# Performance work log

Measured on AMD Instinct MI355X. Metric: run time of the kernel, lower is better.

The kernel has to match this reference:

```python
import jax, jax.numpy as jnp
import numpy as np

EPS = 1e-08


def _l2norm(x):
    return x / (jnp.linalg.norm(x, axis=-1, keepdims=True) + EPS)


def _mlp(x, weights):
    # weights: list of (W, b); gelu between layers, none after last
    n = len(weights)
    for i, (W, b) in enumerate(weights):
        x = x @ W + b
        if i < n - 1:
            x = jax.nn.gelu(x)  # approximate gelu, matches jax.nn.gelu default
    return x


def setup_inputs() -> dict:
    key = jax.random.key(0)
    ks = jax.random.split(key, 16)
    N, A, L, K = 65536, 32, 256, 1024
    enc_dims = [A, 512, 1024, L]
    dec_dims = [L, 1024, 512, A]

    def lin(k, din, dout):
        kw, kb = jax.random.split(k)
        W = jax.random.normal(kw, (din, dout), jnp.float32) / np.sqrt(din)
        b = jnp.zeros((dout,), jnp.float32)
        return W, b

    inp = {}
    inp["action"] = jax.random.normal(ks[0], (N, A), jnp.float32)
    inp["dim_weights"] = jax.random.uniform(ks[1], (A,), jnp.float32)
    for i in range(3):
        W, b = lin(ks[2 + i], enc_dims[i], enc_dims[i + 1])
        inp[f"enc_w{i}"], inp[f"enc_b{i}"] = W, b
    for i in range(3):
        W, b = lin(ks[5 + i], dec_dims[i], dec_dims[i + 1])
        inp[f"dec_w{i}"], inp[f"dec_b{i}"] = W, b
    cb = jax.random.normal(ks[8], (K, L), jnp.float32) * 0.1
    inp["codebook"] = _l2norm(cb)
    return inp


def reference(action, dim_weights,
              enc_w0, enc_b0, enc_w1, enc_b1, enc_w2, enc_b2,
              dec_w0, dec_b0, dec_w1, dec_b1, dec_w2, dec_b2,
              codebook):
    enc = [(enc_w0, enc_b0), (enc_w1, enc_b1), (enc_w2, enc_b2)]
    dec = [(dec_w0, dec_b0), (dec_w1, dec_b1), (dec_w2, dec_b2)]

    z_e = _l2norm(_mlp(action, enc))                       # [N, L]
    cb = _l2norm(codebook)                                 # [K, L]
    # squared euclidean distances [N, K]
    dists = (jnp.sum(z_e * z_e, axis=-1, keepdims=True)
             - 2.0 * z_e @ cb.T
             + jnp.sum(cb * cb, axis=-1))
    code_idx = jnp.argmin(dists, axis=-1)                  # [N]
    z_q = cb[code_idx]                                     # [N, L]

    z_q_ste = z_e + jax.lax.stop_gradient(z_q - z_e)
    action_hat = _mlp(z_q_ste, dec)                        # [N, A]

    sq_err = (action - action_hat) ** 2 * dim_weights
    recon_loss = jnp.mean(sq_err)
    codebook_loss = jnp.mean((jax.lax.stop_gradient(z_e) - z_q) ** 2)
    commit_loss = jnp.mean((z_e - jax.lax.stop_gradient(z_q)) ** 2)
    return action_hat, code_idx, recon_loss, codebook_loss, commit_loss
```

## Files before the change

kernel.cpp:

```cpp
#include <hip/hip_runtime.h>
#include <math.h>

#define N_ROWS 65536

typedef short short8 __attribute__((ext_vector_type(8)));
typedef float f32x4 __attribute__((ext_vector_type(4)));

__device__ __forceinline__ float gelu_f(float x) {
  float x3 = x * x * x;
  float t = tanhf(0.7978845608028654f * (x + 0.044715f * x3));
  return 0.5f * x * (1.0f + t);
}

__device__ __forceinline__ unsigned short f2bf(float f) {
  unsigned u = __float_as_uint(f);
  unsigned r = u + 0x7fffu + ((u >> 16) & 1u);
  return (unsigned short)(r >> 16);
}
__device__ __forceinline__ float bf2f(unsigned short h) {
  return __uint_as_float(((unsigned)h) << 16);
}

__device__ __forceinline__ void split3(float v, unsigned short& p0,
                                       unsigned short& p1, unsigned short& p2) {
  p0 = f2bf(v);
  float r = v - bf2f(p0);
  p1 = f2bf(r);
  r -= bf2f(p1);
  p2 = f2bf(r);
}

__device__ __forceinline__ void split3f(float v, unsigned short& p0,
                                        unsigned short& p1, unsigned short& p2) {
  unsigned u = __float_as_uint(v);
  unsigned h0 = (u + 0x8000u) & 0xffff0000u;
  float r = v - __uint_as_float(h0);
  unsigned u1 = __float_as_uint(r);
  unsigned h1 = (u1 + 0x8000u) & 0xffff0000u;
  float r2 = r - __uint_as_float(h1);
  p0 = (unsigned short)(h0 >> 16);
  p1 = (unsigned short)(h1 >> 16);
  p2 = f2bf(r2);
}

__device__ __forceinline__ void split2f(float v, unsigned short& p0,
                                        unsigned short& p1) {
  unsigned u = __float_as_uint(v);
  unsigned h0 = (u + 0x8000u) & 0xffff0000u;
  float r = v - __uint_as_float(h0);
  p0 = (unsigned short)(h0 >> 16);
  p1 = f2bf(r);
}

__device__ __forceinline__ f32x4 mfma16(short8 a, short8 b, f32x4 c) {
  return __builtin_amdgcn_mfma_f32_16x16x32_bf16(a, b, c, 0, 0, 0);
}

__global__ __launch_bounds__(256) void gemm_enc0_split(
    const float* __restrict__ A, const float* __restrict__ W,
    const float* __restrict__ bias, unsigned short* __restrict__ P,
    size_t aps, int din, int dout) {
  __shared__ float As[16][132];
  __shared__ float Ws[16][132];
  int t = threadIdx.x;
  int tx = t & 15, ty = t >> 4;
  int c0 = blockIdx.x * 128;
  int r0 = blockIdx.y * 128;

  float acc[8][8];
#pragma unroll
  for (int i = 0; i < 8; ++i)
#pragma unroll
    for (int j = 0; j < 8; ++j) acc[i][j] = 0.0f;

  int kchunks = din >> 4;
  for (int kc = 0; kc < kchunks; ++kc) {
    int k0 = kc << 4;
    __syncthreads();
#pragma unroll
    for (int it = 0; it < 2; ++it) {
      int id = t + it * 256;
      int r = id >> 2;
      int kq = (id & 3) * 4;
      float4 v = *(const float4*)&A[(long)(r0 + r) * din + (k0 + kq)];
      As[kq + 0][r] = v.x; As[kq + 1][r] = v.y;
      As[kq + 2][r] = v.z; As[kq + 3][r] = v.w;
      int k = id >> 5;
      int cq = (id & 31) * 4;
      float4 w = *(const float4*)&W[(long)(k0 + k) * dout + (c0 + cq)];
      *(float4*)&Ws[k][cq] = w;
    }
    __syncthreads();
#pragma unroll
    for (int k = 0; k < 16; ++k) {
      float av[8], bv[8];
      *(float4*)&av[0] = *(const float4*)&As[k][ty * 4];
      *(float4*)&av[4] = *(const float4*)&As[k][ty * 4 + 64];
      *(float4*)&bv[0] = *(const float4*)&Ws[k][tx * 4];
      *(float4*)&bv[4] = *(const float4*)&Ws[k][tx * 4 + 64];
#pragma unroll
      for (int i = 0; i < 8; ++i)
#pragma unroll
        for (int j = 0; j < 8; ++j)
          acc[i][j] = fmaf(av[i], bv[j], acc[i][j]);
    }
  }

  float bbv[8];
  *(float4*)&bbv[0] = *(const float4*)&bias[c0 + tx * 4];
  *(float4*)&bbv[4] = *(const float4*)&bias[c0 + tx * 4 + 64];
#pragma unroll
  for (int i = 0; i < 8; ++i) {
    long row = r0 + ty * 4 + (i & 3) + ((i >> 2) * 64);
    unsigned short s0[8], s1[8], s2[8];
#pragma unroll
    for (int j = 0; j < 8; ++j) {
      float v = gelu_f(acc[i][j] + bbv[j]);
      split3f(v, s0[j], s1[j], s2[j]);
    }
    size_t b = (size_t)row * dout + c0 + tx * 4;
    ushort4 w;
    w.x = s0[0]; w.y = s0[1]; w.z = s0[2]; w.w = s0[3];
    *(ushort4*)&P[b] = w;
    w.x = s0[4]; w.y = s0[5]; w.z = s0[6]; w.w = s0[7];
    *(ushort4*)&P[b + 64] = w;
    w.x = s1[0]; w.y = s1[1]; w.z = s1[2]; w.w = s1[3];
    *(ushort4*)&P[aps + b] = w;
    w.x = s1[4]; w.y = s1[5]; w.z = s1[6]; w.w = s1[7];
    *(ushort4*)&P[aps + b + 64] = w;
    w.x = s2[0]; w.y = s2[1]; w.z = s2[2]; w.w = s2[3];
    *(ushort4*)&P[2 * aps + b] = w;
    w.x = s2[4]; w.y = s2[5]; w.z = s2[6]; w.w = s2[7];
    *(ushort4*)&P[2 * aps + b + 64] = w;
  }
}

template <bool GELU>
__global__ __launch_bounds__(256) void gemm64_kernel(
    const float* __restrict__ A, const float* __restrict__ W,
    const float* __restrict__ bias, float* __restrict__ C,
    int din, int dout) {
  __shared__ float As[16][68];
  __shared__ float Ws[16][68];
  int t = threadIdx.x;
  int tx = t & 15, ty = t >> 4;
  int c0 = blockIdx.x * 64;
  int r0 = blockIdx.y * 64;

  float acc[4][4];
#pragma unroll
  for (int i = 0; i < 4; ++i)
#pragma unroll
    for (int j = 0; j < 4; ++j) acc[i][j] = 0.0f;

  int kchunks = din >> 4;
  for (int kc = 0; kc < kchunks; ++kc) {
    int k0 = kc << 4;
    __syncthreads();
    {
      int r = t >> 2, kq = (t & 3) * 4;
      float4 v = *(const float4*)&A[(long)(r0 + r) * din + (k0 + kq)];
      As[kq + 0][r] = v.x; As[kq + 1][r] = v.y;
      As[kq + 2][r] = v.z; As[kq + 3][r] = v.w;
      int k = t >> 4, cq = (t & 15) * 4;
      *(float4*)&Ws[k][cq] = *(const float4*)&W[(long)(k0 + k) * dout + (c0 + cq)];
    }
    __syncthreads();
#pragma unroll
    for (int k = 0; k < 16; ++k) {
      float av[4], bv[4];
      *(float4*)&av[0] = *(const float4*)&As[k][ty * 4];
      *(float4*)&bv[0] = *(const float4*)&Ws[k][tx * 4];
#pragma unroll
      for (int i = 0; i < 4; ++i)
#pragma unroll
        for (int j = 0; j < 4; ++j)
          acc[i][j] = fmaf(av[i], bv[j], acc[i][j]);
    }
  }

  float4 bb = *(const float4*)&bias[c0 + tx * 4];
#pragma unroll
  for (int i = 0; i < 4; ++i) {
    long row = r0 + ty * 4 + i;
    float o[4];
    o[0] = acc[i][0] + bb.x; o[1] = acc[i][1] + bb.y;
    o[2] = acc[i][2] + bb.z; o[3] = acc[i][3] + bb.w;
    if (GELU) {
      o[0] = gelu_f(o[0]); o[1] = gelu_f(o[1]);
      o[2] = gelu_f(o[2]); o[3] = gelu_f(o[3]);
    }
    *(float4*)&C[row * dout + c0 + tx * 4] = *(float4*)&o[0];
  }
}

__global__ void frag_pack_kernel(const float* __restrict__ W,
                                 unsigned short* __restrict__ Bf,
                                 int K, int N) {
  int l = threadIdx.x;
  int m = l & 15, q = l >> 4;
  int cb = blockIdx.x, kb = blockIdx.y;
  unsigned short s0[8], s1[8], s2[8];
#pragma unroll
  for (int j = 0; j < 8; ++j) {
    float v = W[(long)(kb * 32 + q * 8 + j) * N + cb * 16 + m];
    split3(v, s0[j], s1[j], s2[j]);
  }
  size_t base = ((size_t)cb * (K / 32) + kb) * 3 * 512;
  *(short8*)&Bf[base + 0 * 512 + l * 8] = *(short8*)s0;
  *(short8*)&Bf[base + 1 * 512 + l * 8] = *(short8*)s1;
  *(short8*)&Bf[base + 2 * 512 + l * 8] = *(short8*)s2;
}

__global__ void frag_pack2_t(const float* __restrict__ cbn,
                             unsigned short* __restrict__ Bf) {
  int l = threadIdx.x;
  int m = l & 15, q = l >> 4;
  int cb = blockIdx.x, kb = blockIdx.y;
  unsigned short s0[8], s1[8];
  const float* src = cbn + (long)(cb * 16 + m) * 256 + kb * 32 + q * 8;
#pragma unroll
  for (int j = 0; j < 8; ++j) split2f(src[j], s0[j], s1[j]);
  size_t base = ((size_t)(cb * 8 + kb) * 2) * 512;
  *(short8*)&Bf[base + l * 8] = *(short8*)s0;
  *(short8*)&Bf[base + 512 + l * 8] = *(short8*)s1;
}

template <bool GELU>
__global__ __launch_bounds__(256) void mfma3_gemm(
    const unsigned short* __restrict__ Ap, size_t aps,
    const unsigned short* __restrict__ Bf,
    const float* __restrict__ bias, float* __restrict__ C,
    int K, int dout) {
  __shared__ unsigned short A_f[2][3 * 2 * 4 * 512];
  int t = threadIdx.x;
  int lane = t & 63, wave = t >> 6;
  int q = lane >> 4, m = lane & 15;
  int wrb = wave >> 1;
  int wr = wrb * 64, wc = (wave & 1) * 64;

  int gx = gridDim.x, tot = gx * gridDim.y;
  int lin = blockIdx.y * gx + blockIdx.x;
  if (!(tot & 7)) lin = (lin & 7) * (tot >> 3) + (lin >> 3);
  int bx = lin % gx, by = lin / gx;

  long r0 = (long)by * 128;
  int c0 = bx * 128;
  int kchunks = K >> 5;

  f32x4 acc[4][4];
#pragma unroll
  for (int i = 0; i < 4; ++i)
#pragma unroll
    for (int j = 0; j < 4; ++j) acc[i][j] = (f32x4){0.f, 0.f, 0.f, 0.f};

  int rs = t >> 1, hs = (t & 1) * 16;
  const unsigned short* a0p = Ap + (size_t)(r0 + rs) * K + hs;
  const unsigned short* a1p = a0p + aps;
  const unsigned short* a2p = a0p + 2 * aps;
  int cb0 = (c0 + wc) >> 4;
  int xw = (rs >> 4) & 3, wrbw = rs >> 6, mw = rs & 15;
  int g0 = ((t & 1) * 2 + 0) * 16 + mw;
  int g1 = ((t & 1) * 2 + 1) * 16 + mw;
  int wb0 = (0 * 2 + wrbw) * 4 + xw;
  int wb1 = (1 * 2 + wrbw) * 4 + xw;
  int wb2 = (2 * 2 + wrbw) * 4 + xw;

  {
    uint4 u00 = *(const uint4*)(a0p);
    uint4 u01 = *(const uint4*)(a0p + 8);
    uint4 u10 = *(const uint4*)(a1p);
    uint4 u11 = *(const uint4*)(a1p + 8);
    uint4 u20 = *(const uint4*)(a2p);
    uint4 u21 = *(const uint4*)(a2p + 8);
    *(uint4*)&A_f[0][wb0 * 512 + g0 * 8] = u00;
    *(uint4*)&A_f[0][wb0 * 512 + g1 * 8] = u01;
    *(uint4*)&A_f[0][wb1 * 512 + g0 * 8] = u10;
    *(uint4*)&A_f[0][wb1 * 512 + g1 * 8] = u11;
    *(uint4*)&A_f[0][wb2 * 512 + g0 * 8] = u20;
    *(uint4*)&A_f[0][wb2 * 512 + g1 * 8] = u21;
  }
  __syncthreads();

  int cur = 0;
  for (int kb = 0; kb < kchunks; ++kb) {
    short8 af[3][4];
#pragma unroll
    for (int p = 0; p < 3; ++p)
#pragma unroll
      for (int x = 0; x < 4; ++x)
        af[p][x] =
            *(const short8*)&A_f[cur][((p * 2 + wrb) * 4 + x) * 512 + lane * 8];
#pragma unroll
    for (int ct = 0; ct < 4; ++ct) {
      size_t fb = ((size_t)(cb0 + ct) * kchunks + kb) * 3 * 512 + lane * 8;
      short8 b0 = *(const short8*)&Bf[fb];
      short8 b1 = *(const short8*)&Bf[fb + 512];
      short8 b2 = *(const short8*)&Bf[fb + 1024];
#pragma unroll
      for (int rt = 0; rt < 4; ++rt) {
        acc[rt][ct] = mfma16(af[0][rt], b0, acc[rt][ct]);
        acc[rt][ct] = mfma16(af[0][rt], b1, acc[rt][ct]);
        acc[rt][ct] = mfma16(af[1][rt], b0, acc[rt][ct]);
        acc[rt][ct] = mfma16(af[0][rt], b2, acc[rt][ct]);
        acc[rt][ct] = mfma16(af[1][rt], b1, acc[rt][ct]);
        acc[rt][ct] = mfma16(af[2][rt], b0, acc[rt][ct]);
      }
    }
    if (kb + 1 < kchunks) {
      int kt = (kb + 1) << 5;
      uint4 u00 = *(const uint4*)(a0p + kt);
      uint4 u01 = *(const uint4*)(a0p + kt + 8);
      uint4 u10 = *(const uint4*)(a1p + kt);
      uint4 u11 = *(const uint4*)(a1p + kt + 8);
      uint4 u20 = *(const uint4*)(a2p + kt);
      uint4 u21 = *(const uint4*)(a2p + kt + 8);
      int nb = cur ^ 1;
      *(uint4*)&A_f[nb][wb0 * 512 + g0 * 8] = u00;
      *(uint4*)&A_f[nb][wb0 * 512 + g1 * 8] = u01;
      *(uint4*)&A_f[nb][wb1 * 512 + g0 * 8] = u10;
      *(uint4*)&A_f[nb][wb1 * 512 + g1 * 8] = u11;
      *(uint4*)&A_f[nb][wb2 * 512 + g0 * 8] = u20;
      *(uint4*)&A_f[nb][wb2 * 512 + g1 * 8] = u21;
    }
    __syncthreads();
    cur ^= 1;
  }

#pragma unroll
  for (int ct = 0; ct < 4; ++ct) {
    long col = c0 + wc + ct * 16 + m;
    float bv = bias[col];
#pragma unroll
    for (int rt = 0; rt < 4; ++rt) {
      long rowb = r0 + wr + rt * 16 + q * 4;
#pragma unroll
      for (int r = 0; r < 4; ++r) {
        float v = acc[rt][ct][r] + bv;
        if (GELU) v = gelu_f(v);
        C[(rowb + r) * dout + col] = v;
      }
    }
  }
}

__global__ __launch_bounds__(256) void mfma3_norm(
    const float* __restrict__ A, const unsigned short* __restrict__ Bf,
    const float* __restrict__ bias, float* __restrict__ z_e,
    float* __restrict__ ze2) {
  __shared__ unsigned short A_f[2][3 * 4 * 512];
  __shared__ float S[64][4];
  __shared__ float Sinv[64];
  const int K = 1024, kchunks = 32;
  int t = threadIdx.x;
  int lane = t & 63, wave = t >> 6;
  int q = lane >> 4, m = lane & 15;
  long r0 = (long)blockIdx.x * 64;

  f32x4 acc[4][4];
#pragma unroll
  for (int i = 0; i < 4; ++i)
#pragma unroll
    for (int j = 0; j < 4; ++j) acc[i][j] = (f32x4){0.f, 0.f, 0.f, 0.f};

  int rs = t >> 2, kq = t & 3;
  const float* aptr = A + (r0 + rs) * K + kq * 8;
  int xw = rs >> 4, mw = rs & 15;
  int gw = kq * 16 + mw;
  int wb0 = 0 * 4 + xw, wb1 = 1 * 4 + xw, wb2 = 2 * 4 + xw;
  int cb0 = wave * 4;

  {
    float fv[8];
    *(float4*)&fv[0] = *(const float4*)(aptr);
    *(float4*)&fv[4] = *(const float4*)(aptr + 4);
    unsigned short a0[8], a1[8], a2[8];
#pragma unroll
    for (int i = 0; i < 8; ++i) split3f(fv[i], a0[i], a1[i], a2[i]);
    *(uint4*)&A_f[0][wb0 * 512 + gw * 8] = *(uint4*)a0;
    *(uint4*)&A_f[0][wb1 * 512 + gw * 8] = *(uint4*)a1;
    *(uint4*)&A_f[0][wb2 * 512 + gw * 8] = *(uint4*)a2;
  }
  __syncthreads();

  int cur = 0;
  for (int kb = 0; kb < kchunks; ++kb) {
    short8 af[3][4];
#pragma unroll
    for (int p = 0; p < 3; ++p)
#pragma unroll
      for (int x = 0; x < 4; ++x)
        af[p][x] = *(const short8*)&A_f[cur][(p * 4 + x) * 512 + lane * 8];
#pragma unroll
    for (int ct = 0; ct < 4; ++ct) {
      size_t fb = ((size_t)(cb0 + ct) * kchunks + kb) * 3 * 512 + lane * 8;
      short8 b0 = *(const short8*)&Bf[fb];
      short8 b1 = *(const short8*)&Bf[fb + 512];
      short8 b2 = *(const short8*)&Bf[fb + 1024];
#pragma unroll
      for (int rt = 0; rt < 4; ++rt) {
        acc[rt][ct] = mfma16(af[0][rt], b0, acc[rt][ct]);
        acc[rt][ct] = mfma16(af[0][rt], b1, acc[rt][ct]);
        acc[rt][ct] = mfma16(af[1][rt], b0, acc[rt][ct]);
        acc[rt][ct] = mfma16(af[0][rt], b2, acc[rt][ct]);
        acc[rt][ct] = mfma16(af[1][rt], b1, acc[rt][ct]);
        acc[rt][ct] = mfma16(af[2][rt], b0, acc[rt][ct]);
      }
    }
    if (kb + 1 < kchunks) {
      float fv[8];
      *(float4*)&fv[0] = *(const float4*)(aptr + ((kb + 1) << 5));
      *(float4*)&fv[4] = *(const float4*)(aptr + ((kb + 1) << 5) + 4);
      unsigned short a0[8], a1[8], a2[8];
#pragma unroll
      for (int i = 0; i < 8; ++i) split3f(fv[i], a0[i], a1[i], a2[i]);
      int nb = cur ^ 1;
      *(uint4*)&A_f[nb][wb0 * 512 + gw * 8] = *(uint4*)a0;
      *(uint4*)&A_f[nb][wb1 * 512 + gw * 8] = *(uint4*)a1;
      *(uint4*)&A_f[nb][wb2 * 512 + gw * 8] = *(uint4*)a2;
    }
    __syncthreads();
    cur ^= 1;
  }

#pragma unroll
  for (int ct = 0; ct < 4; ++ct) {
    float bv = bias[wave * 64 + ct * 16 + m];
#pragma unroll
    for (int rt = 0; rt < 4; ++rt)
#pragma unroll
      for (int r = 0; r < 4; ++r) acc[rt][ct][r] += bv;
  }

#pragma unroll
  for (int rt = 0; rt < 4; ++rt)
#pragma unroll
    for (int r = 0; r < 4; ++r) {
      float s = acc[rt][0][r] * acc[rt][0][r] + acc[rt][1][r] * acc[rt][1][r] +
                acc[rt][2][r] * acc[rt][2][r] + acc[rt][3][r] * acc[rt][3][r];
#pragma unroll
      for (int off = 1; off <= 8; off <<= 1) s += __shfl_xor(s, off);
      if (m == 0) S[rt * 16 + q * 4 + r][wave] = s;
    }
  __syncthreads();
  if (t < 64) {
    float s = S[t][0] + S[t][1] + S[t][2] + S[t][3];
    float den = sqrtf(s) + 1e-8f;
    Sinv[t] = 1.0f / den;
    ze2[r0 + t] = s / (den * den);
  }
  __syncthreads();
#pragma unroll
  for (int rt = 0; rt < 4; ++rt)
#pragma unroll
    for (int r = 0; r < 4; ++r) {
      int rl = rt * 16 + q * 4 + r;
      float inv = Sinv[rl];
#pragma unroll
      for (int ct = 0; ct < 4; ++ct)
        z_e[(r0 + rl) * 256 + wave * 64 + ct * 16 + m] = acc[rt][ct][r] * inv;
    }
}

__global__ __launch_bounds__(256) void dist2_mfma(
    const float* __restrict__ z_e, const unsigned short* __restrict__ cbf,
    int* __restrict__ idxc, int* __restrict__ fixcnt, int* __restrict__ fixlist) {
  __shared__ unsigned short A_f[2 * 8 * 4 * 512];
  __shared__ float Lv1[64][4], Lv2[64][4];
  __shared__ int Lc1[64][4];
  int t = threadIdx.x;
  int lane = t & 63, wave = t >> 6;
  int q = lane >> 4, m = lane & 15;
  long r0 = (long)blockIdx.x * 64;

#pragma unroll
  for (int it = 0; it < 4; ++it) {
    int kb = it * 2 + (t >> 7);
    int rs = (t & 127) >> 1, hs = (t & 1) * 16;
    const float* ap = z_e + (r0 + rs) * 256 + kb * 32 + hs;
    float fv[16];
    *(float4*)&fv[0] = *(const float4*)(ap + 0);
    *(float4*)&fv[4] = *(const float4*)(ap + 4);
    *(float4*)&fv[8] = *(const float4*)(ap + 8);
    *(float4*)&fv[12] = *(const float4*)(ap + 12);
    unsigned short a0[16], a1[16];
#pragma unroll
    for (int i = 0; i < 16; ++i) split2f(fv[i], a0[i], a1[i]);
    int x = rs >> 4, mm = rs & 15;
    int ga = ((t & 1) * 2 + 0) * 16 + mm;
    int gb = ((t & 1) * 2 + 1) * 16 + mm;
    int b0 = ((0 * 8 + kb) * 4 + x) * 512;
    int b1 = ((1 * 8 + kb) * 4 + x) * 512;
    *(uint4*)&A_f[b0 + ga * 8] = ((uint4*)a0)[0];
    *(uint4*)&A_f[b0 + gb * 8] = ((uint4*)a0)[1];
    *(uint4*)&A_f[b1 + ga * 8] = ((uint4*)a1)[0];
    *(uint4*)&A_f[b1 + gb * 8] = ((uint4*)a1)[1];
  }
  __syncthreads();

  float v1[4][4], v2[4][4];
  int c1[4][4];
#pragma unroll
  for (int i = 0; i < 4; ++i)
#pragma unroll
    for (int j = 0; j < 4; ++j) { v1[i][j] = -3.4e38f; v2[i][j] = -3.4e38f; c1[i][j] = 0; }

  for (int ctp = 0; ctp < 4; ++ctp) {
    f32x4 acc[4][4];
#pragma unroll
    for (int i = 0; i < 4; ++i)
#pragma unroll
      for (int j = 0; j < 4; ++j) acc[i][j] = (f32x4){0.f, 0.f, 0.f, 0.f};

    for (int kb = 0; kb < 8; ++kb) {
      short8 af0[4], af1[4];
#pragma unroll
      for (int rt = 0; rt < 4; ++rt) {
        af0[rt] = *(const short8*)&A_f[((0 * 8 + kb) * 4 + rt) * 512 + lane * 8];
        af1[rt] = *(const short8*)&A_f[((1 * 8 + kb) * 4 + rt) * 512 + lane * 8];
      }
      short8 bf0[4], bf1[4];
#pragma unroll
      for (int cs = 0; cs < 4; ++cs) {
        int cb = ctp * 16 + (cs >> 1) * 8 + wave * 2 + (cs & 1);
        size_t fb = ((size_t)(cb * 8 + kb) * 2) * 512 + lane * 8;
        bf0[cs] = *(const short8*)&cbf[fb];
        bf1[cs] = *(const short8*)&cbf[fb + 512];
      }
#pragma unroll
      for (int rt = 0; rt < 4; ++rt)
#pragma unroll
        for (int cs = 0; cs < 4; ++cs) {
          acc[rt][cs] = mfma16(af0[rt], bf0[cs], acc[rt][cs]);
          acc[rt][cs] = mfma16(af0[rt], bf1[cs], acc[rt][cs]);
          acc[rt][cs] = mfma16(af1[rt], bf0[cs], acc[rt][cs]);
        }
    }
#pragma unroll
    for (int rt = 0; rt < 4; ++rt)
#pragma unroll
      for (int cs = 0; cs < 4; ++cs) {
        int colb = ctp * 256 + (cs >> 1) * 128 + wave * 32 + (cs & 1) * 16 + m;
#pragma unroll
        for (int r = 0; r < 4; ++r) {
          float v = acc[rt][cs][r];
          float nv2 = fmaxf(v2[rt][r], fminf(v, v1[rt][r]));
          if (v > v1[rt][r]) { c1[rt][r] = colb; v1[rt][r] = v; }
          v2[rt][r] = nv2;
        }
      }
  }

#pragma unroll
  for (int off = 1; off <= 8; off <<= 1) {
#pragma unroll
    for (int rt = 0; rt < 4; ++rt)
#pragma unroll
      for (int r = 0; r < 4; ++r) {
        float ov1 = __shfl_xor(v1[rt][r], off);
        float ov2 = __shfl_xor(v2[rt][r], off);
        int oc1 = __shfl_xor(c1[rt][r], off);
        float nv2 = fmaxf(fmaxf(v2[rt][r], ov2), fminf(v1[rt][r], ov1));
        if (ov1 > v1[rt][r] || (ov1 == v1[rt][r] && oc1 < c1[rt][r])) {
          v1[rt][r] = ov1; c1[rt][r] = oc1;
        }
        v2[rt][r] = nv2;
      }
  }
  if (m == 0) {
#pragma unroll
    for (int rt = 0; rt < 4; ++rt)
#pragma unroll
      for (int r = 0; r < 4; ++r) {
        int rloc = rt * 16 + q * 4 + r;
        Lv1[rloc][wave] = v1[rt][r];
        Lv2[rloc][wave] = v2[rt][r];
        Lc1[rloc][wave] = c1[rt][r];
      }
  }
  __syncthreads();
  if (t < 64) {
    float a1 = Lv1[t][0], a2 = Lv2[t][0];
    int ac = Lc1[t][0];
#pragma unroll
    for (int w = 1; w < 4; ++w) {
      float b1 = Lv1[t][w], b2 = Lv2[t][w];
      int bc = Lc1[t][w];
      float n2 = fmaxf(fmaxf(a2, b2), fminf(a1, b1));
      if (b1 > a1 || (b1 == a1 && bc < ac)) { a1 = b1; ac = bc; }
      a2 = n2;
    }
    idxc[r0 + t] = ac;
    if (a1 - a2 < 5.0e-4f) {
      int p = atomicAdd(fixcnt, 1);
      fixlist[p] = r0 + t;
    }
  }
}

__global__ __launch_bounds__(256) void fixup_part(
    const float* __restrict__ z_e, const float* __restrict__ cbn,
    const float* __restrict__ ze2, const float* __restrict__ cb2,
    const int* __restrict__ fixlist, const int* __restrict__ fixcnt,
    float* __restrict__ fixbv, int* __restrict__ fixbc) {
  int cnt = *fixcnt;
  int r0 = blockIdx.y * 128;
  if (r0 >= cnt) return;
  int ctile = blockIdx.x;
  int c0 = ctile * 128;
  __shared__ float As[16][132];
  __shared__ float Ws[16][132];
  __shared__ float rv[128][17];
  __shared__ int rc[128][17];
  __shared__ int rows_l[128];
  int t = threadIdx.x, tx = t & 15, ty = t >> 4;

  if (t < 128) rows_l[t] = fixlist[(r0 + t < cnt) ? (r0 + t) : 0];
  __syncthreads();

  float bestv[8];
  int bestc[8];
  float myze2[8];
#pragma unroll
  for (int i = 0; i < 8; ++i) {
    bestv[i] = 3.4e38f;
    bestc[i] = 0;
    int rl = ty * 4 + (i & 3) + ((i >> 2) * 64);
    myze2[i] = ze2[rows_l[rl]];
  }

  float acc[8][8];
#pragma unroll
  for (int i = 0; i < 8; ++i)
#pragma unroll
    for (int j = 0; j < 8; ++j) acc[i][j] = 0.0f;

  for (int kc = 0; kc < 16; ++kc) {
    int k0 = kc << 4;
    __syncthreads();
#pragma unroll
    for (int it = 0; it < 2; ++it) {
      int id = t + it * 256;
      int r = id >> 2;
      int kq = (id & 3) * 4;
      float4 v = *(const float4*)&z_e[(long)rows_l[r] * 256 + k0 + kq];
      As[kq + 0][r] = v.x; As[kq + 1][r] = v.y;
      As[kq + 2][r] = v.z; As[kq + 3][r] = v.w;
      float4 w = *(const float4*)&cbn[(long)(c0 + r) * 256 + k0 + kq];
      Ws[kq + 0][r] = w.x; Ws[kq + 1][r] = w.y;
      Ws[kq + 2][r] = w.z; Ws[kq + 3][r] = w.w;
    }
    __syncthreads();
#pragma unroll
    for (int k = 0; k < 16; ++k) {
      float av[8], bv[8];
      *(float4*)&av[0] = *(const float4*)&As[k][ty * 4];
      *(float4*)&av[4] = *(const float4*)&As[k][ty * 4 + 64];
      *(float4*)&bv[0] = *(const float4*)&Ws[k][tx * 4];
      *(float4*)&bv[4] = *(const float4*)&Ws[k][tx * 4 + 64];
#pragma unroll
      for (int i = 0; i < 8; ++i)
#pragma unroll
        for (int j = 0; j < 8; ++j)
          acc[i][j] = fmaf(av[i], bv[j], acc[i][j]);
    }
  }

  float cb2v[8];
  *(float4*)&cb2v[0] = *(const float4*)&cb2[c0 + tx * 4];
  *(float4*)&cb2v[4] = *(const float4*)&cb2[c0 + tx * 4 + 64];
#pragma unroll
  for (int i = 0; i < 8; ++i)
#pragma unroll
    for (int j = 0; j < 8; ++j) {
      int c = c0 + tx * 4 + (j & 3) + ((j >> 2) * 64);
      float d = (myze2[i] - 2.0f * acc[i][j]) + cb2v[j];
      if (d < bestv[i] || (d == bestv[i] && c < bestc[i])) {
        bestv[i] = d;
        bestc[i] = c;
      }
    }

  __syncthreads();
#pragma unroll
  for (int i = 0; i < 8; ++i) {
    int rl = ty * 4 + (i & 3) + ((i >> 2) * 64);
    rv[rl][tx] = bestv[i];
    rc[rl][tx] = bestc[i];
  }
  __syncthreads();
  if (t < 128 && r0 + t < cnt) {
    float bv = rv[t][0];
    int bc = rc[t][0];
    for (int j = 1; j < 16; ++j) {
      float v = rv[t][j];
      int c = rc[t][j];
      if (v < bv || (v == bv && c < bc)) { bv = v; bc = c; }
    }
    fixbv[(long)(r0 + t) * 8 + ctile] = bv;
    fixbc[(long)(r0 + t) * 8 + ctile] = bc;
  }
}

__global__ __launch_bounds__(256) void fixup_reduce(
    const float* __restrict__ fixbv, const int* __restrict__ fixbc,
    const int* __restrict__ fixlist, const int* __restrict__ fixcnt,
    int* __restrict__ idxc) {
  int cnt = *fixcnt;
  int i = blockIdx.x * 256 + threadIdx.x;
  if (i >= cnt) return;
  float bv = fixbv[(long)i * 8];
  int bc = fixbc[(long)i * 8];
#pragma unroll
  for (int j = 1; j < 8; ++j) {
    float v = fixbv[(long)i * 8 + j];
    int c = fixbc[(long)i * 8 + j];
    if (v < bv || (v == bv && c < bc)) { bv = v; bc = c; }
  }
  idxc[fixlist[i]] = bc;
}

__global__ __launch_bounds__(256) void rownorm_kernel(
    const float* __restrict__ in, float* __restrict__ outv,
    float* __restrict__ outsq) {
  int wid = threadIdx.x >> 6, lane = threadIdx.x & 63;
  long row = (long)blockIdx.x * 4 + wid;
  const float* src = in + row * 256;
  float4 v = *(const float4*)&src[lane * 4];
  float s = v.x * v.x + v.y * v.y + v.z * v.z + v.w * v.w;
#pragma unroll
  for (int off = 32; off >= 1; off >>= 1) s += __shfl_xor(s, off);
  float denom = sqrtf(s) + 1e-8f;
  float4 o;
  o.x = v.x / denom; o.y = v.y / denom; o.z = v.z / denom; o.w = v.w / denom;
  *(float4*)&outv[row * 256 + lane * 4] = o;
  float s2 = o.x * o.x + o.y * o.y + o.z * o.z + o.w * o.w;
#pragma unroll
  for (int off = 32; off >= 1; off >>= 1) s2 += __shfl_xor(s2, off);
  if (lane == 0) outsq[row] = s2;
}

__global__ __launch_bounds__(256) void t2_kernel(
    const float* __restrict__ T1, const float* __restrict__ W,
    const float* __restrict__ bias, float* __restrict__ T2) {
  int id = blockIdx.x * 256 + threadIdx.x;
  int row = id >> 5, col = id & 31;
  const float* a = T1 + (long)row * 512;
  float s = 0.f;
#pragma unroll 8
  for (int k = 0; k < 512; ++k) s = fmaf(a[k], W[k * 32 + col], s);
  T2[id] = s + bias[col];
}

__global__ __launch_bounds__(256) void fused_tail(
    const float* __restrict__ z_e, const float* __restrict__ cbn,
    const int* __restrict__ idxc, const float* __restrict__ T2,
    const float* __restrict__ action, const float* __restrict__ dimw,
    float* __restrict__ partRe, float* __restrict__ partCo,
    float* __restrict__ outIdx, float* __restrict__ ahat, int pb) {
  int t = threadIdx.x, wid = t >> 6, lane = t & 63;
  float cs = 0.f, rsum = 0.f;
#pragma unroll
  for (int r = 0; r < 4; ++r) {
    long row = (long)blockIdx.x * 16 + wid * 4 + r;
    int k = idxc[row];
    float4 a = *(const float4*)&z_e[row * 256 + lane * 4];
    float4 b = *(const float4*)&cbn[(long)k * 256 + lane * 4];
    float dx = a.x - b.x, dy = a.y - b.y, dz = a.z - b.z, dq = a.w - b.w;
    cs += dx * dx + dy * dy + dz * dz + dq * dq;
    if (lane < 8) {
      float4 av = *(const float4*)&action[row * 32 + lane * 4];
      float4 tv = *(const float4*)&T2[(long)k * 32 + lane * 4];
      float4 wv = *(const float4*)&dimw[lane * 4];
      *(float4*)&ahat[row * 32 + lane * 4] = tv;
      float ex = av.x - tv.x, ey = av.y - tv.y;
      float ez = av.z - tv.z, ew = av.w - tv.w;
      rsum += ex * ex * wv.x + ey * ey * wv.y + ez * ez * wv.z + ew * ew * wv.w;
    }
    if (lane == 0) outIdx[row] = (float)k;
  }
#pragma unroll
  for (int off = 32; off >= 1; off >>= 1) {
    cs += __shfl_xor(cs, off);
    rsum += __shfl_xor(rsum, off);
  }
  __shared__ float rc[4], rr[4];
  if (lane == 0) { rc[wid] = cs; rr[wid] = rsum; }
  __syncthreads();
  if (t == 0) {
    partCo[pb + blockIdx.x] = rc[0] + rc[1] + rc[2] + rc[3];
    partRe[pb + blockIdx.x] = rr[0] + rr[1] + rr[2] + rr[3];
  }
}

__global__ void zero_kernel(int* __restrict__ cnts) {
  if (threadIdx.x < 32) cnts[threadIdx.x] = 0;
}

__global__ __launch_bounds__(256) void finalize_kernel(
    const float* __restrict__ partRe, const float* __restrict__ partCo,
    float* __restrict__ out) {
  int t = threadIdx.x;
  float sr = 0.f, sc = 0.f;
  for (int i = t; i < 4096; i += 256) { sr += partRe[i]; sc += partCo[i]; }
#pragma unroll
  for (int off = 32; off >= 1; off >>= 1) {
    sr += __shfl_xor(sr, off);
    sc += __shfl_xor(sc, off);
  }
  __shared__ float rs_[4], cs_[4];
  int wid = t >> 6, lane = t & 63;
  if (lane == 0) { rs_[wid] = sr; cs_[wid] = sc; }
  __syncthreads();
  if (t == 0) {
    float r = rs_[0] + rs_[1] + rs_[2] + rs_[3];
    float c = cs_[0] + cs_[1] + cs_[2] + cs_[3];
    out[0] = r / (65536.0f * 32.0f);
    float cl = c / (65536.0f * 256.0f);
    out[1] = cl;
    out[2] = cl;
  }
}

extern "C" void kernel_launch(void* const* d_in, const int* in_sizes, int n_in,
                              void* d_out, int out_size, void* d_ws,
                              size_t ws_size, hipStream_t stream) {
  const float* action = (const float*)d_in[0];
  const float* dimw = (const float*)d_in[1];
  const float* ew0 = (const float*)d_in[2];
  const float* eb0 = (const float*)d_in[3];
  const float* ew1 = (const float*)d_in[4];
  const float* eb1 = (const float*)d_in[5];
  const float* ew2 = (const float*)d_in[6];
  const float* eb2 = (const float*)d_in[7];
  const float* dw0 = (const float*)d_in[8];
  const float* db0 = (const float*)d_in[9];
  const float* dw1 = (const float*)d_in[10];
  const float* db1 = (const float*)d_in[11];
  const float* dw2 = (const float*)d_in[12];
  const float* db2 = (const float*)d_in[13];
  const float* cb = (const float*)d_in[14];
  float* out = (float*)d_out;
  char* ws = (char*)d_ws;

  const size_t fixed_b = 1048576 + 4096 + 1048576 + 3145728 + 1572864 +
                         4194304 + 2097152 + 131072 + 256 + 32768;
  int R = N_ROWS;
  while (R > 2048) {
    if (fixed_b + (size_t)R * 7244 + 65536 <= ws_size) break;
    R >>= 1;
  }

  size_t off = 0;
  float* cbn = (float*)(ws + off); off += 1048576;
  float* cb2 = (float*)(ws + off); off += 4096;
  unsigned short* cbf = (unsigned short*)(ws + off); off += 1048576;
  unsigned short* ewf1 = (unsigned short*)(ws + off); off += 3145728;
  unsigned short* ewf2 = (unsigned short*)(ws + off); off += 1572864;
  float* T0 = (float*)(ws + off); off += 4194304;
  float* T1d = (float*)(ws + off); off += 2097152;
  float* T2d = (float*)(ws + off); off += 131072;
  int* fixcnts = (int*)(ws + off); off += 256;
  float* partRe = (float*)(ws + off); off += 16384;
  float* partCo = (float*)(ws + off); off += 16384;
  float* ze2 = (float*)(ws + off); off += (size_t)R * 4;
  int* idxc = (int*)(ws + off); off += (size_t)R * 4;
  int* fixlist = (int*)(ws + off); off += (size_t)R * 4;
  float* fixbv = (float*)(ws + off); off += (size_t)R * 32;
  int* fixbc = (int*)(ws + off); off += (size_t)R * 32;
  char* P0 = ws + off; off += (size_t)R * 3072;
  char* P1 = ws + off; off += (size_t)R * 4096;

  unsigned short* e0p = (unsigned short*)P0;
  size_t aps0 = (size_t)R * 512;
  float* e1 = (float*)P1;
  float* z_e = (float*)P0;

  zero_kernel<<<1, 64, 0, stream>>>(fixcnts);
  rownorm_kernel<<<256, 256, 0, stream>>>(cb, cbn, cb2);
  frag_pack2_t<<<dim3(64, 8), 64, 0, stream>>>(cbn, cbf);
  frag_pack_kernel<<<dim3(64, 16), 64, 0, stream>>>(ew1, ewf1, 512, 1024);
  frag_pack_kernel<<<dim3(16, 32), 64, 0, stream>>>(ew2, ewf2, 1024, 256);

  gemm64_kernel<true><<<dim3(16, 16), 256, 0, stream>>>(cbn, dw0, db0, T0, 256, 1024);
  gemm64_kernel<true><<<dim3(8, 16), 256, 0, stream>>>(T0, dw1, db1, T1d, 1024, 512);
  t2_kernel<<<128, 256, 0, stream>>>(T1d, dw2, db2, T2d);

  for (int base = 0; base < N_ROWS; base += R) {
    int ci = base / R;
    const float* act_c = action + (size_t)base * 32;
    float* out_c = out + (size_t)base * 32;
    int* fixcnt = &fixcnts[ci];

    gemm_enc0_split<<<dim3(4, R / 128), 256, 0, stream>>>(
        act_c, ew0, eb0, e0p, aps0, 32, 512);
    mfma3_gemm<true><<<dim3(8, R / 128), 256, 0, stream>>>(
        e0p, aps0, ewf1, eb1, e1, 512, 1024);
    mfma3_norm<<<R / 64, 256, 0, stream>>>(e1, ewf2, eb2, z_e, ze2);

    dist2_mfma<<<R / 64, 256, 0, stream>>>(z_e, cbf, idxc, fixcnt, fixlist);
    fixup_part<<<dim3(8, R / 128), 256, 0, stream>>>(
        z_e, cbn, ze2, cb2, fixlist, fixcnt, fixbv, fixbc);
    fixup_reduce<<<R / 256, 256, 0, stream>>>(fixbv, fixbc, fixlist, fixcnt,
                                              idxc);

    fused_tail<<<R / 16, 256, 0, stream>>>(
        z_e, cbn, idxc, T2d, act_c, dimw, partRe, partCo,
        out + 2097152 + base, out_c, base >> 4);
  }

  finalize_kernel<<<1, 256, 0, stream>>>(partRe, partCo, out + 2162688);
}
```

Baseline: 1.126 ms.

## Prefetch next B fragment in MFMA GEMMs and run VQ stages once over all rows

```diff
diff --git a/kernel.cpp b/kernel.cpp
--- a/kernel.cpp
+++ b/kernel.cpp
@@ -266,6 +266,13 @@
   int wb1 = (1 * 2 + wrbw) * 4 + xw;
   int wb2 = (2 * 2 + wrbw) * 4 + xw;
 
+  short8 pf0, pf1, pf2;
+  {
+    size_t fb = ((size_t)cb0 * kchunks) * 1536 + lane * 8;
+    pf0 = *(const short8*)&Bf[fb];
+    pf1 = *(const short8*)&Bf[fb + 512];
+    pf2 = *(const short8*)&Bf[fb + 1024];
+  }
   {
     uint4 u00 = *(const uint4*)(a0p);
     uint4 u01 = *(const uint4*)(a0p + 8);
@@ -292,8 +299,23 @@
         af[p][x] =
             *(const short8*)&A_f[cur][((p * 2 + wrb) * 4 + x) * 512 + lane * 8];
 #pragma unroll
-    for (int ct = 0; ct < 4; ++ct) {
-      size_t fb = ((size_t)(cb0 + ct) * kchunks + kb) * 3 * 512 + lane * 8;
+    for (int rt = 0; rt < 4; ++rt) {
+      acc[rt][0] = mfma16(af[0][rt], pf0, acc[rt][0]);
+      acc[rt][0] = mfma16(af[0][rt], pf1, acc[rt][0]);
+      acc[rt][0] = mfma16(af[1][rt], pf0, acc[rt][0]);
+      acc[rt][0] = mfma16(af[0][rt], pf2, acc[rt][0]);
+      acc[rt][0] = mfma16(af[1][rt], pf1, acc[rt][0]);
+      acc[rt][0] = mfma16(af[2][rt], pf0, acc[rt][0]);
+    }
+    if (kb + 1 < kchunks) {
+      size_t fb = ((size_t)cb0 * kchunks + kb + 1) * 1536 + lane * 8;
+      pf0 = *(const short8*)&Bf[fb];
+      pf1 = *(const short8*)&Bf[fb + 512];
+      pf2 = *(const short8*)&Bf[fb + 1024];
+    }
+#pragma unroll
+    for (int ct = 1; ct < 4; ++ct) {
+      size_t fb = ((size_t)(cb0 + ct) * kchunks + kb) * 1536 + lane * 8;
       short8 b0 = *(const short8*)&Bf[fb];
       short8 b1 = *(const short8*)&Bf[fb + 512];
       short8 b2 = *(const short8*)&Bf[fb + 1024];
@@ -370,6 +392,13 @@
   int wb0 = 0 * 4 + xw, wb1 = 1 * 4 + xw, wb2 = 2 * 4 + xw;
   int cb0 = wave * 4;
 
+  short8 pf0, pf1, pf2;
+  {
+    size_t fb = ((size_t)cb0 * kchunks) * 1536 + lane * 8;
+    pf0 = *(const short8*)&Bf[fb];
+    pf1 = *(const short8*)&Bf[fb + 512];
+    pf2 = *(const short8*)&Bf[fb + 1024];
+  }
   {
     float fv[8];
     *(float4*)&fv[0] = *(const float4*)(aptr);
@@ -392,8 +421,23 @@
       for (int x = 0; x < 4; ++x)
         af[p][x] = *(const short8*)&A_f[cur][(p * 4 + x) * 512 + lane * 8];
 #pragma unroll
-    for (int ct = 0; ct < 4; ++ct) {
-      size_t fb = ((size_t)(cb0 + ct) * kchunks + kb) * 3 * 512 + lane * 8;
+    for (int rt = 0; rt < 4; ++rt) {
+      acc[rt][0] = mfma16(af[0][rt], pf0, acc[rt][0]);
+      acc[rt][0] = mfma16(af[0][rt], pf1, acc[rt][0]);
+      acc[rt][0] = mfma16(af[1][rt], pf0, acc[rt][0]);
+      acc[rt][0] = mfma16(af[0][rt], pf2, acc[rt][0]);
+      acc[rt][0] = mfma16(af[1][rt], pf1, acc[rt][0]);
+      acc[rt][0] = mfma16(af[2][rt], pf0, acc[rt][0]);
+    }
+    if (kb + 1 < kchunks) {
+      size_t fb = ((size_t)cb0 * kchunks + kb + 1) * 1536 + lane * 8;
+      pf0 = *(const short8*)&Bf[fb];
+      pf1 = *(const short8*)&Bf[fb + 512];
+      pf2 = *(const short8*)&Bf[fb + 1024];
+    }
+#pragma unroll
+    for (int ct = 1; ct < 4; ++ct) {
+      size_t fb = ((size_t)(cb0 + ct) * kchunks + kb) * 1536 + lane * 8;
       short8 b0 = *(const short8*)&Bf[fb];
       short8 b1 = *(const short8*)&Bf[fb + 512];
       short8 b2 = *(const short8*)&Bf[fb + 1024];
@@ -757,7 +801,7 @@
     const int* __restrict__ idxc, const float* __restrict__ T2,
     const float* __restrict__ action, const float* __restrict__ dimw,
     float* __restrict__ partRe, float* __restrict__ partCo,
-    float* __restrict__ outIdx, float* __restrict__ ahat, int pb) {
+    float* __restrict__ outIdx, float* __restrict__ ahat) {
   int t = threadIdx.x, wid = t >> 6, lane = t & 63;
   float cs = 0.f, rsum = 0.f;
 #pragma unroll
@@ -788,8 +832,8 @@
   if (lane == 0) { rc[wid] = cs; rr[wid] = rsum; }
   __syncthreads();
   if (t == 0) {
-    partCo[pb + blockIdx.x] = rc[0] + rc[1] + rc[2] + rc[3];
-    partRe[pb + blockIdx.x] = rr[0] + rr[1] + rr[2] + rr[3];
+    partCo[blockIdx.x] = rc[0] + rc[1] + rc[2] + rc[3];
+    partRe[blockIdx.x] = rr[0] + rr[1] + rr[2] + rr[3];
   }
 }
 
@@ -845,9 +889,10 @@
 
   const size_t fixed_b = 1048576 + 4096 + 1048576 + 3145728 + 1572864 +
                          4194304 + 2097152 + 131072 + 256 + 32768;
+  const size_t full_b = (size_t)N_ROWS * 1024 + (size_t)N_ROWS * 4;
   int R = N_ROWS;
   while (R > 2048) {
-    if (fixed_b + (size_t)R * 7244 + 65536 <= ws_size) break;
+    if (fixed_b + full_b + (size_t)R * 7168 + 65536 <= ws_size) break;
     R >>= 1;
   }
 
@@ -863,18 +908,18 @@
   int* fixcnts = (int*)(ws + off); off += 256;
   float* partRe = (float*)(ws + off); off += 16384;
   float* partCo = (float*)(ws + off); off += 16384;
-  float* ze2 = (float*)(ws + off); off += (size_t)R * 4;
-  int* idxc = (int*)(ws + off); off += (size_t)R * 4;
-  int* fixlist = (int*)(ws + off); off += (size_t)R * 4;
-  float* fixbv = (float*)(ws + off); off += (size_t)R * 32;
-  int* fixbc = (int*)(ws + off); off += (size_t)R * 32;
+  float* z_e = (float*)(ws + off); off += (size_t)N_ROWS * 1024;
+  float* ze2 = (float*)(ws + off); off += (size_t)N_ROWS * 4;
   char* P0 = ws + off; off += (size_t)R * 3072;
   char* P1 = ws + off; off += (size_t)R * 4096;
 
   unsigned short* e0p = (unsigned short*)P0;
   size_t aps0 = (size_t)R * 512;
   float* e1 = (float*)P1;
-  float* z_e = (float*)P0;
+  int* idxc = (int*)P1;
+  int* fixlist = (int*)(P1 + 262144);
+  float* fixbv = (float*)(P1 + 524288);
+  int* fixbc = (int*)(P1 + 524288 + 2097152);
 
   zero_kernel<<<1, 64, 0, stream>>>(fixcnts);
   rownorm_kernel<<<256, 256, 0, stream>>>(cb, cbn, cb2);
@@ -887,27 +932,23 @@
   t2_kernel<<<128, 256, 0, stream>>>(T1d, dw2, db2, T2d);
 
   for (int base = 0; base < N_ROWS; base += R) {
-    int ci = base / R;
     const float* act_c = action + (size_t)base * 32;
-    float* out_c = out + (size_t)base * 32;
-    int* fixcnt = &fixcnts[ci];
-
     gemm_enc0_split<<<dim3(4, R / 128), 256, 0, stream>>>(
         act_c, ew0, eb0, e0p, aps0, 32, 512);
     mfma3_gemm<true><<<dim3(8, R / 128), 256, 0, stream>>>(
         e0p, aps0, ewf1, eb1, e1, 512, 1024);
-    mfma3_norm<<<R / 64, 256, 0, stream>>>(e1, ewf2, eb2, z_e, ze2);
-
-    dist2_mfma<<<R / 64, 256, 0, stream>>>(z_e, cbf, idxc, fixcnt, fixlist);
-    fixup_part<<<dim3(8, R / 128), 256, 0, stream>>>(
-        z_e, cbn, ze2, cb2, fixlist, fixcnt, fixbv, fixbc);
-    fixup_reduce<<<R / 256, 256, 0, stream>>>(fixbv, fixbc, fixlist, fixcnt,
-                                              idxc);
-
-    fused_tail<<<R / 16, 256, 0, stream>>>(
-        z_e, cbn, idxc, T2d, act_c, dimw, partRe, partCo,
-        out + 2097152 + base, out_c, base >> 4);
-  }
+    mfma3_norm<<<R / 64, 256, 0, stream>>>(e1, ewf2, eb2,
+                                           z_e + (size_t)base * 256, ze2 + base);
+  }
+
+  dist2_mfma<<<N_ROWS / 64, 256, 0, stream>>>(z_e, cbf, idxc, &fixcnts[0],
+                                              fixlist);
+  fixup_part<<<dim3(8, N_ROWS / 128), 256, 0, stream>>>(
+      z_e, cbn, ze2, cb2, fixlist, &fixcnts[0], fixbv, fixbc);
+  fixup_reduce<<<N_ROWS / 256, 256, 0, stream>>>(fixbv, fixbc, fixlist,
+                                                 &fixcnts[0], idxc);
+  fused_tail<<<N_ROWS / 16, 256, 0, stream>>>(
+      z_e, cbn, idxc, T2d, action, dimw, partRe, partCo, out + 2097152, out);
 
   finalize_kernel<<<1, 256, 0, stream>>>(partRe, partCo, out + 2162688);
 }
```

New measurement: 1.255 ms. +11.4%, slower.

## Split dist2 codebook columns across eight waves and reduce top-2 per tile

Applied to the files above, without the earlier changes.

```diff
diff --git a/kernel.cpp b/kernel.cpp
--- a/kernel.cpp
+++ b/kernel.cpp
@@ -462,20 +462,24 @@
     }
 }
 
-__global__ __launch_bounds__(256) void dist2_mfma(
+__global__ __launch_bounds__(512) void dist2_mfma(
     const float* __restrict__ z_e, const unsigned short* __restrict__ cbf,
     int* __restrict__ idxc, int* __restrict__ fixcnt, int* __restrict__ fixlist) {
   __shared__ unsigned short A_f[2 * 8 * 4 * 512];
-  __shared__ float Lv1[64][4], Lv2[64][4];
-  __shared__ int Lc1[64][4];
+  __shared__ float Lv1[64][8], Lv2[64][8];
+  __shared__ int Lc1[64][8];
   int t = threadIdx.x;
   int lane = t & 63, wave = t >> 6;
   int q = lane >> 4, m = lane & 15;
   long r0 = (long)blockIdx.x * 64;
 
-#pragma unroll
-  for (int it = 0; it < 4; ++it) {
-    int kb = it * 2 + (t >> 7);
+  Lv1[t >> 3][t & 7] = -3.4e38f;
+  Lv2[t >> 3][t & 7] = -3.4e38f;
+  Lc1[t >> 3][t & 7] = 0;
+
+#pragma unroll
+  for (int it = 0; it < 2; ++it) {
+    int kb = it * 4 + (t >> 7);
     int rs = (t & 127) >> 1, hs = (t & 1) * 16;
     const float* ap = z_e + (r0 + rs) * 256 + kb * 32 + hs;
     float fv[16];
@@ -498,92 +502,76 @@
   }
   __syncthreads();
 
-  float v1[4][4], v2[4][4];
-  int c1[4][4];
-#pragma unroll
-  for (int i = 0; i < 4; ++i)
-#pragma unroll
-    for (int j = 0; j < 4; ++j) { v1[i][j] = -3.4e38f; v2[i][j] = -3.4e38f; c1[i][j] = 0; }
-
   for (int ctp = 0; ctp < 4; ++ctp) {
-    f32x4 acc[4][4];
-#pragma unroll
-    for (int i = 0; i < 4; ++i)
-#pragma unroll
-      for (int j = 0; j < 4; ++j) acc[i][j] = (f32x4){0.f, 0.f, 0.f, 0.f};
+    f32x4 acc[4][2];
+#pragma unroll
+    for (int i = 0; i < 4; ++i) {
+      acc[i][0] = (f32x4){0.f, 0.f, 0.f, 0.f};
+      acc[i][1] = (f32x4){0.f, 0.f, 0.f, 0.f};
+    }
 
     for (int kb = 0; kb < 8; ++kb) {
-      short8 af0[4], af1[4];
-#pragma unroll
-      for (int rt = 0; rt < 4; ++rt) {
-        af0[rt] = *(const short8*)&A_f[((0 * 8 + kb) * 4 + rt) * 512 + lane * 8];
-        af1[rt] = *(const short8*)&A_f[((1 * 8 + kb) * 4 + rt) * 512 + lane * 8];
-      }
-      short8 bf0[4], bf1[4];
-#pragma unroll
-      for (int cs = 0; cs < 4; ++cs) {
-        int cb = ctp * 16 + (cs >> 1) * 8 + wave * 2 + (cs & 1);
+      short8 bf0[2], bf1[2];
+#pragma unroll
+      for (int cs = 0; cs < 2; ++cs) {
+        int cb = ctp * 16 + wave * 2 + cs;
         size_t fb = ((size_t)(cb * 8 + kb) * 2) * 512 + lane * 8;
         bf0[cs] = *(const short8*)&cbf[fb];
         bf1[cs] = *(const short8*)&cbf[fb + 512];
       }
 #pragma unroll
-      for (int rt = 0; rt < 4; ++rt)
-#pragma unroll
-        for (int cs = 0; cs < 4; ++cs) {
-          acc[rt][cs] = mfma16(af0[rt], bf0[cs], acc[rt][cs]);
-          acc[rt][cs] = mfma16(af0[rt], bf1[cs], acc[rt][cs]);
-          acc[rt][cs] = mfma16(af1[rt], bf0[cs], acc[rt][cs]);
-        }
-    }
-#pragma unroll
-    for (int rt = 0; rt < 4; ++rt)
-#pragma unroll
-      for (int cs = 0; cs < 4; ++cs) {
-        int colb = ctp * 256 + (cs >> 1) * 128 + wave * 32 + (cs & 1) * 16 + m;
-#pragma unroll
-        for (int r = 0; r < 4; ++r) {
-          float v = acc[rt][cs][r];
-          float nv2 = fmaxf(v2[rt][r], fminf(v, v1[rt][r]));
-          if (v > v1[rt][r]) { c1[rt][r] = colb; v1[rt][r] = v; }
-          v2[rt][r] = nv2;
+      for (int rt = 0; rt < 4; ++rt) {
+        short8 a0 = *(const short8*)&A_f[((0 * 8 + kb) * 4 + rt) * 512 + lane * 8];
+        short8 a1 = *(const short8*)&A_f[((1 * 8 + kb) * 4 + rt) * 512 + lane * 8];
+#pragma unroll
+        for (int cs = 0; cs < 2; ++cs) {
+          acc[rt][cs] = mfma16(a0, bf0[cs], acc[rt][cs]);
+          acc[rt][cs] = mfma16(a0, bf1[cs], acc[rt][cs]);
+          acc[rt][cs] = mfma16(a1, bf0[cs], acc[rt][cs]);
         }
       }
-  }
-
-#pragma unroll
-  for (int off = 1; off <= 8; off <<= 1) {
-#pragma unroll
-    for (int rt = 0; rt < 4; ++rt)
+    }
+
+    int colb0 = ctp * 256 + wave * 32 + m;
+#pragma unroll
+    for (int rt = 0; rt < 4; ++rt) {
 #pragma unroll
       for (int r = 0; r < 4; ++r) {
-        float ov1 = __shfl_xor(v1[rt][r], off);
-        float ov2 = __shfl_xor(v2[rt][r], off);
-        int oc1 = __shfl_xor(c1[rt][r], off);
-        float nv2 = fmaxf(fmaxf(v2[rt][r], ov2), fminf(v1[rt][r], ov1));
-        if (ov1 > v1[rt][r] || (ov1 == v1[rt][r] && oc1 < c1[rt][r])) {
-          v1[rt][r] = ov1; c1[rt][r] = oc1;
+        float va = acc[rt][0][r], vb = acc[rt][1][r];
+        float v1l, v2l;
+        int c1l;
+        if (va >= vb) { v1l = va; c1l = colb0; v2l = vb; }
+        else { v1l = vb; c1l = colb0 + 16; v2l = va; }
+#pragma unroll
+        for (int off = 1; off <= 8; off <<= 1) {
+          float ov1 = __shfl_xor(v1l, off);
+          float ov2 = __shfl_xor(v2l, off);
+          int oc1 = __shfl_xor(c1l, off);
+          float nv2 = fmaxf(fmaxf(v2l, ov2), fminf(v1l, ov1));
+          if (ov1 > v1l || (ov1 == v1l && oc1 < c1l)) { v1l = ov1; c1l = oc1; }
+          v2l = nv2;
         }
-        v2[rt][r] = nv2;
+        if (m == 0) {
+          int row = rt * 16 + q * 4 + r;
+          float o1 = Lv1[row][wave], o2 = Lv2[row][wave];
+          int oc = Lc1[row][wave];
+          float n2 = fmaxf(fmaxf(o2, v2l), fminf(o1, v1l));
+          if (v1l > o1 || (v1l == o1 && c1l < oc)) {
+            Lv1[row][wave] = v1l;
+            Lc1[row][wave] = c1l;
+          }
+          Lv2[row][wave] = n2;
+        }
       }
-  }
-  if (m == 0) {
-#pragma unroll
-    for (int rt = 0; rt < 4; ++rt)
-#pragma unroll
-      for (int r = 0; r < 4; ++r) {
-        int rloc = rt * 16 + q * 4 + r;
-        Lv1[rloc][wave] = v1[rt][r];
-        Lv2[rloc][wave] = v2[rt][r];
-        Lc1[rloc][wave] = c1[rt][r];
-      }
-  }
+    }
+  }
+
   __syncthreads();
   if (t < 64) {
     float a1 = Lv1[t][0], a2 = Lv2[t][0];
     int ac = Lc1[t][0];
 #pragma unroll
-    for (int w = 1; w < 4; ++w) {
+    for (int w = 1; w < 8; ++w) {
       float b1 = Lv1[t][w], b2 = Lv2[t][w];
       int bc = Lc1[t][w];
       float n2 = fmaxf(fmaxf(a2, b2), fminf(a1, b1));
@@ -898,7 +886,7 @@
         e0p, aps0, ewf1, eb1, e1, 512, 1024);
     mfma3_norm<<<R / 64, 256, 0, stream>>>(e1, ewf2, eb2, z_e, ze2);
 
-    dist2_mfma<<<R / 64, 256, 0, stream>>>(z_e, cbf, idxc, fixcnt, fixlist);
+    dist2_mfma<<<R / 64, 512, 0, stream>>>(z_e, cbf, idxc, fixcnt, fixlist);
     fixup_part<<<dim3(8, R / 128), 256, 0, stream>>>(
         z_e, cbn, ze2, cb2, fixlist, fixcnt, fixbv, fixbc);
     fixup_reduce<<<R / 256, 256, 0, stream>>>(fixbv, fixbc, fixlist, fixcnt,
```

Result: slower. 1.275 ms (+13.2%).
